# Kernel tuning notes

Measured on AMD Instinct MI355X. Metric: run time of the kernel, lower is better.

The kernel has to match this reference:

```python
import jax, jax.numpy as jnp
import numpy as np

L = 4          # num_levels
N = 32768      # memory slots per level
D_S, D_E, D_C, D_K, D_V, D_Z = 1024, 1024, 512, 128, 512, 128
THR = 0.1      # sparse_write_threshold
EPS = 1e-5


def setup_inputs() -> dict:
    key = jax.random.key(0)
    ks = jax.random.split(key, 16)
    w = lambda k, shape, s=0.02: jax.random.normal(k, shape, dtype=jnp.float32) * s
    return {
        "s_t": jax.random.normal(ks[0], (D_S,), dtype=jnp.float32),
        "e_t": jax.random.normal(ks[1], (D_E,), dtype=jnp.float32),
        "level_contexts": jax.random.normal(ks[2], (L, D_C), dtype=jnp.float32),
        "M": jax.random.normal(ks[3], (L, N, D_V), dtype=jnp.float32) * 0.1,
        "K_mem": jax.random.normal(ks[4], (L, N, D_K), dtype=jnp.float32) * 0.1,
        "decay": jnp.full((L,), 0.01, dtype=jnp.float32),
        "W1_0": w(ks[5], (D_Z, D_S + D_E)),
        "b1_0": jnp.zeros((D_Z,), jnp.float32),
        "W1_r": w(ks[6], (L - 1, D_Z, D_S + D_C + D_E)),
        "b1_r": jnp.zeros((L - 1, D_Z), jnp.float32),
        "spec_wr": w(ks[7], (L, 1, D_Z), 1.0),
        "spec_wi": w(ks[8], (L, 1, D_Z), 1.0),
        "ln_g": jnp.ones((L, D_Z), jnp.float32),
        "ln_b": jnp.zeros((L, D_Z), jnp.float32),
        "Wg": w(ks[9], (L, 1, D_Z), 0.5),
        "bg": jnp.zeros((L, 1), jnp.float32),
        "Wv": w(ks[10], (L, D_V, D_Z)),
        "bv": jnp.zeros((L, D_V), jnp.float32),
        "Wk": w(ks[11], (L, D_K, D_Z)),
        "bk": jnp.zeros((L, D_K), jnp.float32),
    }


def _level_update(ell, x, M, K_mem, decay, W1, b1, spec_wr, spec_wi,
                  ln_g, ln_b, Wg, bg, Wv, bv, Wk, bk):
    # Linear -> SpectralBlock (seq_len=1 FFT filter) -> LayerNorm
    h = W1 @ x + b1                                  # [d_z]
    X = jnp.fft.rfft(h[None, :], axis=0)             # [1, d_z] complex
    Y = X * (spec_wr[ell] + 1j * spec_wi[ell])       # learned spectral filter
    y = jnp.fft.irfft(Y, n=1, axis=0)[0]             # [d_z]
    mu = y.mean()
    var = ((y - mu) ** 2).mean()
    z = (y - mu) * jax.lax.rsqrt(var + EPS) * ln_g[ell] + ln_b[ell]

    g = jax.nn.sigmoid(Wg[ell] @ z + bg[ell])[0]     # scalar write gate
    v = jnp.tanh(Wv[ell] @ z + bv[ell])              # [d_v]
    k = Wk[ell] @ z + bk[ell]                        # [d_k]

    scores = (K_mem[ell] @ k) / np.sqrt(D_K).astype(np.float32)  # [N]
    alpha = jax.nn.softmax(scores)                   # [N]

    # sparse-write branch: if g < threshold, no write (pure decay)
    wgt = jnp.where(g >= THR, g, jnp.float32(0.0))
    keep = (1.0 - decay[ell])
    M_new = keep * M[ell] + wgt * alpha[:, None] * v[None, :]      # [N, d_v]
    K_new = keep * K_mem[ell] + wgt * alpha[:, None] * k[None, :]  # [N, d_k]
    return jnp.concatenate([M_new, K_new], axis=-1)  # [N, d_v + d_k]


def reference(s_t, e_t, level_contexts, M, K_mem, decay, W1_0, b1_0, W1_r, b1_r,
              spec_wr, spec_wi, ln_g, ln_b, Wg, bg, Wv, bv, Wk, bk):
    outs = []
    for ell in range(L):
        if ell == 0:
            x = jnp.concatenate([s_t, e_t])
            W1, b1 = W1_0, b1_0
        else:
            x = jnp.concatenate([s_t, level_contexts[ell - 1], e_t])
            W1, b1 = W1_r[ell - 1], b1_r[ell - 1]
        outs.append(_level_update(ell, x, M, K_mem, decay, W1, b1, spec_wr,
                                  spec_wi, ln_g, ln_b, Wg, bg, Wv, bv, Wk, bk))
    return jnp.stack(outs)  # [L, N, d_v + d_k]
```

## Files before the change

### kernel.cpp

```cpp
#include <hip/hip_runtime.h>
#include <hip/hip_bf16.h>
#include <math.h>

#define NLVL 4
#define NSLOT 32768
#define SB 128

typedef float f4 __attribute__((ext_vector_type(4)));

__global__ __launch_bounds__(256) void k_h(
    const float* __restrict__ s_t, const float* __restrict__ e_t,
    const float* __restrict__ ctx,
    const float* __restrict__ W1_0, const float* __restrict__ b1_0,
    const float* __restrict__ W1_r, const float* __restrict__ b1_r,
    const float* __restrict__ spec_wr, float* __restrict__ ybuf)
{
    const int row = blockIdx.x;
    const int ell = blockIdx.y;
    const int tid = threadIdx.x;
    const int d = (ell == 0) ? 2048 : 2560;
    const float* W1 = (ell == 0) ? W1_0 : (W1_r + (size_t)(ell - 1) * 128 * 2560);
    const float* b1 = (ell == 0) ? b1_0 : (b1_r + (ell - 1) * 128);
    const f4* wrow = (const f4*)(W1 + (size_t)row * d);

    float acc = 0.f;
    if (ell == 0) {
        for (int i4 = tid; i4 < 512; i4 += 256) {
            f4 w = wrow[i4];
            f4 x = (i4 < 256) ? ((const f4*)s_t)[i4]
                              : ((const f4*)e_t)[i4 - 256];
            acc += w.x * x.x + w.y * x.y + w.z * x.z + w.w * x.w;
        }
    } else {
        const f4* c4 = (const f4*)(ctx + (size_t)(ell - 1) * 512);
        for (int i4 = tid; i4 < 640; i4 += 256) {
            f4 w = wrow[i4];
            f4 x;
            if (i4 < 256)      x = ((const f4*)s_t)[i4];
            else if (i4 < 384) x = c4[i4 - 256];
            else               x = ((const f4*)e_t)[i4 - 384];
            acc += w.x * x.x + w.y * x.y + w.z * x.z + w.w * x.w;
        }
    }
    __shared__ float red[256];
    red[tid] = acc;
    __syncthreads();
    for (int off = 128; off > 0; off >>= 1) {
        if (tid < off) red[tid] += red[tid + off];
        __syncthreads();
    }
    if (tid == 0)
        ybuf[ell * 128 + row] = (red[0] + b1[row]) * spec_wr[ell * 128 + row];
}

__global__ __launch_bounds__(256) void k_zvk(
    const float* __restrict__ ybuf,
    const float* __restrict__ ln_g, const float* __restrict__ ln_b,
    const float* __restrict__ Wg, const float* __restrict__ bg,
    const float* __restrict__ decay,
    const float* __restrict__ Wv, const float* __restrict__ bv,
    const float* __restrict__ Wk, const float* __restrict__ bk,
    float* __restrict__ vvec, float* __restrict__ kvec,
    float* __restrict__ wgt, float* __restrict__ keepb)
{
    const int ell = blockIdx.y;
    const int t = threadIdx.x;
    __shared__ float red[128];
    __shared__ float sz[128];

    float y = 0.f;
    if (t < 128) { y = ybuf[ell * 128 + t]; red[t] = y; }
    __syncthreads();
    for (int off = 64; off > 0; off >>= 1) {
        if (t < off) red[t] += red[t + off];
        __syncthreads();
    }
    float mu = red[0] * (1.f / 128.f);
    __syncthreads();
    float dd = y - mu;
    if (t < 128) red[t] = dd * dd;
    __syncthreads();
    for (int off = 64; off > 0; off >>= 1) {
        if (t < off) red[t] += red[t + off];
        __syncthreads();
    }
    float rstd = rsqrtf(red[0] * (1.f / 128.f) + 1e-5f);
    __syncthreads();
    if (t < 128) sz[t] = dd * rstd * ln_g[ell * 128 + t] + ln_b[ell * 128 + t];
    __syncthreads();
    if (t < 128) red[t] = Wg[ell * 128 + t] * sz[t];
    __syncthreads();
    for (int off = 64; off > 0; off >>= 1) {
        if (t < off) red[t] += red[t + off];
        __syncthreads();
    }
    if (t == 0 && blockIdx.x == 0) {
        float g = 1.f / (1.f + expf(-(red[0] + bg[ell])));
        wgt[ell] = (g >= 0.1f) ? g : 0.f;
        keepb[ell] = 1.f - decay[ell];
    }

    const int r = blockIdx.x * 64 + (t >> 2);
    const int lane = t & 3;
    const float* wrow;
    float bias;
    float* outp;
    bool is_v = (r < 512);
    if (is_v) {
        wrow = Wv + ((size_t)ell * 512 + r) * 128;
        bias = bv[ell * 512 + r];
        outp = vvec + ell * 512 + r;
    } else {
        int rk = r - 512;
        wrow = Wk + ((size_t)ell * 128 + rk) * 128;
        bias = bk[ell * 128 + rk];
        outp = kvec + ell * 128 + rk;
    }
    float a = 0.f;
    const f4* w4 = (const f4*)wrow + lane * 8;
    const float* z0 = sz + lane * 32;
    #pragma unroll
    for (int j = 0; j < 8; ++j) {
        f4 w = w4[j];
        a += w.x * z0[j * 4] + w.y * z0[j * 4 + 1] + w.z * z0[j * 4 + 2] + w.w * z0[j * 4 + 3];
    }
    a += __shfl_xor(a, 1);
    a += __shfl_xor(a, 2);
    if (lane == 0) {
        float val = a + bias;
        if (is_v) val = tanhf(val);
        *outp = val;
    }
}

__global__ __launch_bounds__(256) void k_scores(
    const float* __restrict__ K_mem, const float* __restrict__ kvec,
    float* __restrict__ expsc, float* __restrict__ partial)
{
    const int ell = blockIdx.y;
    const int tid = threadIdx.x;
    __shared__ float sk[128];
    __shared__ float red[256];
    if (tid < 128) sk[tid] = kvec[ell * 128 + tid];
    __syncthreads();

    const int n0 = blockIdx.x * (NSLOT / SB);
    const int gid = tid >> 4, lane = tid & 15;
    const float* z0 = sk + lane * 8;
    const float scale = 0.08838834764831845f;
    float acc = 0.f;
    for (int it = 0; it < 16; ++it) {
        int n = n0 + it * 16 + gid;
        const f4* kr = (const f4*)(K_mem + ((size_t)ell * NSLOT + n) * 128) + lane * 2;
        f4 wa = kr[0], wb = kr[1];
        float a = wa.x * z0[0] + wa.y * z0[1] + wa.z * z0[2] + wa.w * z0[3]
                + wb.x * z0[4] + wb.y * z0[5] + wb.z * z0[6] + wb.w * z0[7];
        #pragma unroll
        for (int m = 1; m < 16; m <<= 1) a += __shfl_xor(a, m);
        if (lane == 0) {
            float e = expf(a * scale);
            expsc[(size_t)ell * NSLOT + n] = e;
            acc += e;
        }
    }
    red[tid] = acc;
    __syncthreads();
    for (int off = 128; off > 0; off >>= 1) {
        if (tid < off) red[tid] += red[tid + off];
        __syncthreads();
    }
    if (tid == 0) partial[ell * SB + blockIdx.x] = red[0];
}

__global__ __launch_bounds__(256) void k_write3(
    const float* __restrict__ M, const float* __restrict__ K_mem,
    const float* __restrict__ expsc, const float* __restrict__ partial,
    const float* __restrict__ wgt, const float* __restrict__ keepb,
    const float* __restrict__ vvec, const float* __restrict__ kvec,
    f4* __restrict__ out)
{
    const int b = blockIdx.x;
    const int tid = threadIdx.x;
    const int ell = b >> 9;
    const int r0 = b << 6;

    __shared__ float scoef[64];
    __shared__ f4 sv4[128];
    __shared__ f4 skv4[32];
    __shared__ float red[128];

    if (tid < 128) {
        sv4[tid] = ((const f4*)vvec)[ell * 128 + tid];
        red[tid] = partial[ell * SB + tid];
    } else if (tid < 160) {
        skv4[tid - 128] = ((const f4*)kvec)[ell * 32 + (tid - 128)];
    }
    __syncthreads();
    for (int off = 64; off > 0; off >>= 1) {
        if (tid < off) red[tid] += red[tid + off];
        __syncthreads();
    }
    const float scl = wgt[ell] / red[0];
    const float keep = keepb[ell];
    if (tid < 64) scoef[tid] = expsc[r0 + tid] * scl;
    __syncthreads();

    int dr[5], dj[5];
    bool ism[5];
    #pragma unroll
    for (int k2 = 0; k2 < 5; ++k2) {
        int pos = tid + k2 * 256;
        dr[k2] = pos / 160;
        dj[k2] = pos - dr[k2] * 160;
        ism[k2] = (dj[k2] < 128);
    }

    const size_t ob = (size_t)r0 * 160;
    for (int mi = 0; mi < 8; ++mi) {
        f4 in[5];
        #pragma unroll
        for (int k2 = 0; k2 < 5; ++k2) {
            size_t grow = (size_t)(r0 + mi * 8 + dr[k2]);
            if (ism[k2]) {
                in[k2] = __builtin_nontemporal_load((const f4*)M + grow * 128 + dj[k2]);
            } else {
                in[k2] = ((const f4*)K_mem)[grow * 32 + (dj[k2] - 128)];
            }
        }
        #pragma unroll
        for (int k2 = 0; k2 < 5; ++k2) {
            float c = scoef[mi * 8 + dr[k2]];
            f4 src = ism[k2] ? sv4[dj[k2]] : skv4[dj[k2] - 128];
            f4 o;
            o.x = keep * in[k2].x + c * src.x;
            o.y = keep * in[k2].y + c * src.y;
            o.z = keep * in[k2].z + c * src.z;
            o.w = keep * in[k2].w + c * src.w;
            __builtin_nontemporal_store(o, out + ob + mi * 1280 + tid + k2 * 256);
        }
    }
}

extern "C" void kernel_launch(void* const* d_in, const int* in_sizes, int n_in,
                              void* d_out, int out_size, void* d_ws, size_t ws_size,
                              hipStream_t stream) {
    const float* s_t    = (const float*)d_in[0];
    const float* e_t    = (const float*)d_in[1];
    const float* ctx    = (const float*)d_in[2];
    const float* M      = (const float*)d_in[3];
    const float* K_mem  = (const float*)d_in[4];
    const float* decay  = (const float*)d_in[5];
    const float* W1_0   = (const float*)d_in[6];
    const float* b1_0   = (const float*)d_in[7];
    const float* W1_r   = (const float*)d_in[8];
    const float* b1_r   = (const float*)d_in[9];
    const float* spec_wr= (const float*)d_in[10];
    const float* ln_g   = (const float*)d_in[12];
    const float* ln_b   = (const float*)d_in[13];
    const float* Wg     = (const float*)d_in[14];
    const float* bg     = (const float*)d_in[15];
    const float* Wv     = (const float*)d_in[16];
    const float* bv     = (const float*)d_in[17];
    const float* Wk     = (const float*)d_in[18];
    const float* bk     = (const float*)d_in[19];

    float* ws = (float*)d_ws;
    float* expsc   = ws;
    float* partial = ws + 131072;
    float* ybuf    = ws + 131584;
    float* kvec    = ws + 132096;
    float* vvec    = ws + 132608;
    float* wgt     = ws + 134656;
    float* keepb   = ws + 134660;

    dim3 gh(128, NLVL);
    k_h<<<gh, 256, 0, stream>>>(s_t, e_t, ctx, W1_0, b1_0, W1_r, b1_r,
                                spec_wr, ybuf);

    dim3 gzvk(10, NLVL);
    k_zvk<<<gzvk, 256, 0, stream>>>(ybuf, ln_g, ln_b, Wg, bg, decay,
                                    Wv, bv, Wk, bk, vvec, kvec, wgt, keepb);

    dim3 gs(SB, NLVL);
    k_scores<<<gs, 256, 0, stream>>>(K_mem, kvec, expsc, partial);

    k_write3<<<2048, 256, 0, stream>>>(M, K_mem, expsc, partial, wgt, keepb,
                                       vvec, kvec, (f4*)d_out);
}
```

Before: 147.9 us.

## Widen score grid, pair row loads, split write kernel into M and K passes

The scores kernel now launches 512 blocks per level instead of 128, each covering 64 slots, and every 16-lane group handles two rows at once to keep more loads in flight. The write kernel drops the per-element div/mod mapping of the 160-wide interleaved layout. It instead streams the M part and the K part as two separate contiguous passes, and reduces the 512 partial sums. Workspace offsets move to fit the larger partial array. In exchange, the output stores become row-strided rather than fully contiguous per block, and there are more, smaller score blocks.

```diff
diff --git a/kernel.cpp b/kernel.cpp
--- a/kernel.cpp
+++ b/kernel.cpp
@@ -4,7 +4,7 @@
 
 #define NLVL 4
 #define NSLOT 32768
-#define SB 128
+#define SB 512
 
 typedef float f4 __attribute__((ext_vector_type(4)));
 
@@ -144,23 +144,31 @@
     if (tid < 128) sk[tid] = kvec[ell * 128 + tid];
     __syncthreads();
 
-    const int n0 = blockIdx.x * (NSLOT / SB);
+    const int n0 = blockIdx.x * 64;
     const int gid = tid >> 4, lane = tid & 15;
     const float* z0 = sk + lane * 8;
     const float scale = 0.08838834764831845f;
     float acc = 0.f;
-    for (int it = 0; it < 16; ++it) {
-        int n = n0 + it * 16 + gid;
-        const f4* kr = (const f4*)(K_mem + ((size_t)ell * NSLOT + n) * 128) + lane * 2;
-        f4 wa = kr[0], wb = kr[1];
-        float a = wa.x * z0[0] + wa.y * z0[1] + wa.z * z0[2] + wa.w * z0[3]
-                + wb.x * z0[4] + wb.y * z0[5] + wb.z * z0[6] + wb.w * z0[7];
-        #pragma unroll
-        for (int m = 1; m < 16; m <<= 1) a += __shfl_xor(a, m);
+    #pragma unroll
+    for (int it = 0; it < 2; ++it) {
+        int nA = n0 + it * 32 + gid;
+        int nB = nA + 16;
+        const f4* ka = (const f4*)K_mem + ((size_t)ell * NSLOT + nA) * 32 + lane * 2;
+        const f4* kb = (const f4*)K_mem + ((size_t)ell * NSLOT + nB) * 32 + lane * 2;
+        f4 a0 = ka[0], a1 = ka[1];
+        f4 b0 = kb[0], b1 = kb[1];
+        float a = a0.x * z0[0] + a0.y * z0[1] + a0.z * z0[2] + a0.w * z0[3]
+                + a1.x * z0[4] + a1.y * z0[5] + a1.z * z0[6] + a1.w * z0[7];
+        float b = b0.x * z0[0] + b0.y * z0[1] + b0.z * z0[2] + b0.w * z0[3]
+                + b1.x * z0[4] + b1.y * z0[5] + b1.z * z0[6] + b1.w * z0[7];
+        #pragma unroll
+        for (int m = 1; m < 16; m <<= 1) { a += __shfl_xor(a, m); b += __shfl_xor(b, m); }
         if (lane == 0) {
-            float e = expf(a * scale);
-            expsc[(size_t)ell * NSLOT + n] = e;
-            acc += e;
+            float ea = expf(a * scale);
+            float eb = expf(b * scale);
+            expsc[(size_t)ell * NSLOT + nA] = ea;
+            expsc[(size_t)ell * NSLOT + nB] = eb;
+            acc += ea + eb;
         }
     }
     red[tid] = acc;
@@ -172,7 +180,7 @@
     if (tid == 0) partial[ell * SB + blockIdx.x] = red[0];
 }
 
-__global__ __launch_bounds__(256) void k_write3(
+__global__ __launch_bounds__(256) void k_write4(
     const float* __restrict__ M, const float* __restrict__ K_mem,
     const float* __restrict__ expsc, const float* __restrict__ partial,
     const float* __restrict__ wgt, const float* __restrict__ keepb,
@@ -187,16 +195,13 @@
     __shared__ float scoef[64];
     __shared__ f4 sv4[128];
     __shared__ f4 skv4[32];
-    __shared__ float red[128];
-
-    if (tid < 128) {
-        sv4[tid] = ((const f4*)vvec)[ell * 128 + tid];
-        red[tid] = partial[ell * SB + tid];
-    } else if (tid < 160) {
-        skv4[tid - 128] = ((const f4*)kvec)[ell * 32 + (tid - 128)];
-    }
-    __syncthreads();
-    for (int off = 64; off > 0; off >>= 1) {
+    __shared__ float red[256];
+
+    if (tid < 128) sv4[tid] = ((const f4*)vvec)[ell * 128 + tid];
+    if (tid < 32)  skv4[tid] = ((const f4*)kvec)[ell * 32 + tid];
+    red[tid] = partial[ell * SB + tid] + partial[ell * SB + 256 + tid];
+    __syncthreads();
+    for (int off = 128; off > 0; off >>= 1) {
         if (tid < off) red[tid] += red[tid + off];
         __syncthreads();
     }
@@ -205,38 +210,51 @@
     if (tid < 64) scoef[tid] = expsc[r0 + tid] * scl;
     __syncthreads();
 
-    int dr[5], dj[5];
-    bool ism[5];
-    #pragma unroll
-    for (int k2 = 0; k2 < 5; ++k2) {
-        int pos = tid + k2 * 256;
-        dr[k2] = pos / 160;
-        dj[k2] = pos - dr[k2] * 160;
-        ism[k2] = (dj[k2] < 128);
-    }
-
-    const size_t ob = (size_t)r0 * 160;
-    for (int mi = 0; mi < 8; ++mi) {
-        f4 in[5];
-        #pragma unroll
-        for (int k2 = 0; k2 < 5; ++k2) {
-            size_t grow = (size_t)(r0 + mi * 8 + dr[k2]);
-            if (ism[k2]) {
-                in[k2] = __builtin_nontemporal_load((const f4*)M + grow * 128 + dj[k2]);
-            } else {
-                in[k2] = ((const f4*)K_mem)[grow * 32 + (dj[k2] - 128)];
-            }
-        }
-        #pragma unroll
-        for (int k2 = 0; k2 < 5; ++k2) {
-            float c = scoef[mi * 8 + dr[k2]];
-            f4 src = ism[k2] ? sv4[dj[k2]] : skv4[dj[k2] - 128];
+    const size_t obase = (size_t)r0 * 160;
+    const f4* Mb = (const f4*)M + (size_t)r0 * 128;
+    const f4* Kb = (const f4*)K_mem + (size_t)r0 * 32;
+
+    for (int t8 = 0; t8 < 8; ++t8) {
+        f4 in[4];
+        int idx[4];
+        #pragma unroll
+        for (int j = 0; j < 4; ++j) {
+            idx[j] = t8 * 1024 + j * 256 + tid;
+            in[j] = __builtin_nontemporal_load(Mb + idx[j]);
+        }
+        #pragma unroll
+        for (int j = 0; j < 4; ++j) {
+            int row = idx[j] >> 7, col = idx[j] & 127;
+            float c = scoef[row];
+            f4 s = sv4[col];
             f4 o;
-            o.x = keep * in[k2].x + c * src.x;
-            o.y = keep * in[k2].y + c * src.y;
-            o.z = keep * in[k2].z + c * src.z;
-            o.w = keep * in[k2].w + c * src.w;
-            __builtin_nontemporal_store(o, out + ob + mi * 1280 + tid + k2 * 256);
+            o.x = keep * in[j].x + c * s.x;
+            o.y = keep * in[j].y + c * s.y;
+            o.z = keep * in[j].z + c * s.z;
+            o.w = keep * in[j].w + c * s.w;
+            __builtin_nontemporal_store(o, out + obase + (size_t)row * 160 + col);
+        }
+    }
+
+    for (int t8 = 0; t8 < 2; ++t8) {
+        f4 in[4];
+        int idx[4];
+        #pragma unroll
+        for (int j = 0; j < 4; ++j) {
+            idx[j] = t8 * 1024 + j * 256 + tid;
+            in[j] = Kb[idx[j]];
+        }
+        #pragma unroll
+        for (int j = 0; j < 4; ++j) {
+            int row = idx[j] >> 5, col = idx[j] & 31;
+            float c = scoef[row];
+            f4 s = skv4[col];
+            f4 o;
+            o.x = keep * in[j].x + c * s.x;
+            o.y = keep * in[j].y + c * s.y;
+            o.z = keep * in[j].z + c * s.z;
+            o.w = keep * in[j].w + c * s.w;
+            __builtin_nontemporal_store(o, out + obase + (size_t)row * 160 + 128 + col);
         }
     }
 }
@@ -267,11 +285,11 @@
     float* ws = (float*)d_ws;
     float* expsc   = ws;
     float* partial = ws + 131072;
-    float* ybuf    = ws + 131584;
-    float* kvec    = ws + 132096;
-    float* vvec    = ws + 132608;
-    float* wgt     = ws + 134656;
-    float* keepb   = ws + 134660;
+    float* ybuf    = ws + 133120;
+    float* kvec    = ws + 133632;
+    float* vvec    = ws + 134144;
+    float* wgt     = ws + 136192;
+    float* keepb   = ws + 136196;
 
     dim3 gh(128, NLVL);
     k_h<<<gh, 256, 0, stream>>>(s_t, e_t, ctx, W1_0, b1_0, W1_r, b1_r,
@@ -284,6 +302,6 @@
     dim3 gs(SB, NLVL);
     k_scores<<<gs, 256, 0, stream>>>(K_mem, kvec, expsc, partial);
 
-    k_write3<<<2048, 256, 0, stream>>>(M, K_mem, expsc, partial, wgt, keepb,
+    k_write4<<<2048, 256, 0, stream>>>(M, K_mem, expsc, partial, wgt, keepb,
                                        vvec, kvec, (f4*)d_out);
 }
```

Measured after the change: 143.1 us, median of 2. 1.03x faster.
